# Performance work log

Measured on AMD Instinct MI355X. Metric: run time of the kernel, lower is better.

The kernel has to match this reference:

```python
import jax, jax.numpy as jnp
import numpy as np

B, N, C = 4, 2048, 1024
H = 16
D = C // H  # head_dim = 64

def setup_inputs() -> dict:
    key = jax.random.key(0)
    k1, k2, k3 = jax.random.split(key, 3)
    s = 1.0 / np.sqrt(C)
    x = jax.random.normal(k1, (B, N, C), dtype=jnp.float32)
    qkv_w = jax.random.normal(k2, (3 * C, C), dtype=jnp.float32) * s
    proj_w = jax.random.normal(k3, (C, C), dtype=jnp.float32) * s
    proj_b = jnp.zeros((C,), dtype=jnp.float32)
    return {"x": x, "qkv_w": qkv_w, "proj_w": proj_w, "proj_b": proj_b}

def reference(x, qkv_w, proj_w, proj_b):
    # qkv: torch Linear -> x @ W^T, no bias
    qkv = jnp.einsum('bnc,oc->bno', x, qkv_w)            # [B,N,3C]
    qkv = qkv.reshape(B, N, 3, H, D)
    q, k, v = qkv[:, :, 0], qkv[:, :, 1], qkv[:, :, 2]   # [B,N,H,D]
    scale = D ** -0.5
    scores = jnp.einsum('bqhd,bkhd->bhqk', q, k) * scale  # [B,H,N,N]
    causal = jnp.tril(jnp.ones((N, N), dtype=bool))
    scores = jnp.where(causal[None, None], scores, -jnp.inf)
    attn = jax.nn.softmax(scores, axis=-1)
    out = jnp.einsum('bhqk,bkhd->bqhd', attn, v).reshape(B, N, C)
    out = jnp.einsum('bnc,oc->bno', out, proj_w) + proj_b
    return out
```

## Files before the change

kernel.cpp:

```cpp
#include <hip/hip_runtime.h>
#include <math.h>

typedef __attribute__((ext_vector_type(8))) short short8;
typedef __attribute__((ext_vector_type(4))) short short4v;
typedef __attribute__((ext_vector_type(4))) float f32x4;
typedef __attribute__((ext_vector_type(4))) _Float16 half4v;

#define B_  4
#define N_  2048
#define C_  1024
#define H_  16
#define D_  64
#define TC3 3072

__device__ __forceinline__ short f2bf(float f) {
    unsigned u = __builtin_bit_cast(unsigned, f);
    u += 0x7fffu + ((u >> 16) & 1u);
    return (short)(u >> 16);
}

__device__ __forceinline__ half4v pack4h(float a, float b, float cc, float d) {
    auto lo = __builtin_amdgcn_cvt_pkrtz(a, b);
    auto hi = __builtin_amdgcn_cvt_pkrtz(cc, d);
    auto v4 = __builtin_shufflevector(lo, hi, 0, 1, 2, 3);
    return __builtin_bit_cast(half4v, v4);
}

__device__ __forceinline__ void gload16(const void* g, void* l) {
    __builtin_amdgcn_global_load_lds(
        (const __attribute__((address_space(1))) void*)g,
        (__attribute__((address_space(3))) void*)l, 16, 0, 0);
}

__global__ __launch_bounds__(256) void cast_to_bf16(const float* __restrict__ in,
                                                    short* __restrict__ out, int n8) {
    const int i = blockIdx.x * 256 + threadIdx.x;
    if (i >= n8) return;
    const float4 a = ((const float4*)in)[2 * i];
    const float4 b = ((const float4*)in)[2 * i + 1];
    short8 t;
    t[0] = f2bf(a.x); t[1] = f2bf(a.y); t[2] = f2bf(a.z); t[3] = f2bf(a.w);
    t[4] = f2bf(b.x); t[5] = f2bf(b.y); t[6] = f2bf(b.z); t[7] = f2bf(b.w);
    ((short8*)out)[i] = t;
}

#define GK 32

template <int MODE>
__global__ __launch_bounds__(256) void gemm_bf16(const short* __restrict__ A,
                                                 const short* __restrict__ Bw,
                                                 const float* __restrict__ bias,
                                                 short* __restrict__ Qb,
                                                 short* __restrict__ Kb,
                                                 _Float16* __restrict__ Vtb,
                                                 float* __restrict__ Fout,
                                                 int M, int Nn, int K) {
    __shared__ short smem[2 * 128 * GK];
    short* As = smem;
    short* Bs = smem + 128 * GK;

    const int tid = threadIdx.x;
    const int w = tid >> 6;
    const int ln = tid & 63;
    const int wm = w >> 1;
    const int wn = w & 1;
    const int c = ln & 15;
    const int g = ln >> 4;

    const int m0 = blockIdx.y * 128;
    const int n0 = blockIdx.x * 128;

    f32x4 acc[4][4];
#pragma unroll
    for (int m = 0; m < 4; ++m)
#pragma unroll
        for (int n = 0; n < 4; ++n) acc[m][n] = (f32x4){0.f, 0.f, 0.f, 0.f};

    const int lrow = ln >> 2;
    const int lseg = (ln & 3) * 8;

    for (int k0 = 0; k0 < K; k0 += GK) {
#pragma unroll
        for (int j = 0; j < 2; ++j) {
            const int row = w * 32 + j * 16 + lrow;
            gload16(A + (size_t)(m0 + row) * K + k0 + lseg, &As[(w * 32 + j * 16) * GK]);
            gload16(Bw + (size_t)(n0 + row) * K + k0 + lseg, &Bs[(w * 32 + j * 16) * GK]);
        }
        asm volatile("s_waitcnt vmcnt(0)" ::: "memory");
        __syncthreads();

        short8 aF[4], bF[4];
#pragma unroll
        for (int m = 0; m < 4; ++m)
            aF[m] = *(const short8*)&As[(wm * 64 + m * 16 + c) * GK + g * 8];
#pragma unroll
        for (int n = 0; n < 4; ++n)
            bF[n] = *(const short8*)&Bs[(wn * 64 + n * 16 + c) * GK + g * 8];
#pragma unroll
        for (int m = 0; m < 4; ++m)
#pragma unroll
            for (int n = 0; n < 4; ++n)
                acc[m][n] = __builtin_amdgcn_mfma_f32_16x16x32_bf16(aF[m], bF[n], acc[m][n], 0, 0, 0);
        __syncthreads();
    }

    if (MODE == 0) {
        const int mat = n0 >> 10;
        if (mat == 2) {
#pragma unroll
            for (int m = 0; m < 4; ++m) {
                const int row = m0 + wm * 64 + m * 16 + g * 4;
                const int b = row >> 11;
                const int nseq = row & 2047;
#pragma unroll
                for (int n = 0; n < 4; ++n) {
                    const int col = n0 + wn * 64 + n * 16 + c;
                    const int h = (col >> 6) & 15;
                    const int d = col & 63;
                    const half4v p = pack4h(acc[m][n][0], acc[m][n][1],
                                            acc[m][n][2], acc[m][n][3]);
                    *(half4v*)&Vtb[((size_t)(b * 16 + h) * 64 + d) * N_ + nseq] = p;
                }
            }
        } else {
            short* base = (mat == 0) ? Qb : Kb;
#pragma unroll
            for (int p = 0; p < 2; ++p) {
                __syncthreads();
                if (wn == p) {
#pragma unroll
                    for (int m = 0; m < 4; ++m)
#pragma unroll
                        for (int n = 0; n < 4; ++n)
#pragma unroll
                            for (int r = 0; r < 4; ++r)
                                smem[(wm * 64 + m * 16 + g * 4 + r) * 64 +
                                     (((n ^ g) * 16) + c)] = f2bf(acc[m][n][r]);
                }
                __syncthreads();
                const int row = tid >> 1;
                const int col0 = (tid & 1) * 32;
                const int gg = (row >> 2) & 3;
                const int grow = m0 + row;
                const int bb = grow >> 11, nseq = grow & 2047;
                const int h = ((n0 + p * 64) >> 6) & 15;
                short* dst = base + ((size_t)(bb * 16 + h) * N_ + nseq) * D_ + col0;
#pragma unroll
                for (int s16 = 0; s16 < 2; ++s16) {
                    const int Cb = col0 + s16 * 16;
                    const int ls_off = row * 64 + ((((Cb >> 4) ^ gg)) << 4);
                    *(short8*)(dst + s16 * 16) = *(const short8*)&smem[ls_off];
                    *(short8*)(dst + s16 * 16 + 8) = *(const short8*)&smem[ls_off + 8];
                }
            }
        }
    } else {
#pragma unroll
        for (int m = 0; m < 4; ++m) {
            const int row = m0 + wm * 64 + m * 16 + g * 4;
#pragma unroll
            for (int n = 0; n < 4; ++n) {
                const int col = n0 + wn * 64 + n * 16 + c;
                const float bv = bias[col];
#pragma unroll
                for (int r = 0; r < 4; ++r)
                    Fout[(size_t)(row + r) * Nn + col] = acc[m][n][r] + bv;
            }
        }
    }
}


__constant__ unsigned char CH_QT[40] = {0,1,2,3, 4,4, 5,5, 6,6, 7,7,
                                        8,8,8, 9,9,9, 10,10,10, 11,11,11,
                                        12,12,12,12, 13,13,13,13, 14,14,14,14, 15,15,15,15};
__constant__ unsigned char CH_C0[40] = {0,0,0,0, 0,1, 0,1, 0,1, 0,1,
                                        0,1,2, 0,1,2, 0,1,2, 0,1,2,
                                        0,1,2,3, 0,1,2,3, 0,1,2,3, 0,1,2,3};
__constant__ unsigned char CH_BASE[16] = {0,1,2,3,4,6,8,10,12,15,18,21,24,28,32,36};

__device__ __forceinline__ void stage_kv(const short* __restrict__ gK,
                                         const short* __restrict__ gV,
                                         short* KsB, short* VsB,
                                         int kt, int w, int lane) {
    const int sub = lane >> 3;
    const int sseg = (lane & 7) ^ sub;
#pragma unroll
    for (int j = 0; j < 2; ++j) {
        const int R0 = w * 16 + j * 8;
        const int row = R0 + sub;
        gload16(gK + (size_t)(kt * 64 + row) * D_ + sseg * 8, KsB + R0 * 64);
        gload16(gV + (size_t)row * N_ + kt * 64 + sseg * 8, VsB + R0 * 64);
    }
}

__global__ __launch_bounds__(256, 4) void attn_part(const short* __restrict__ Qb,
                                                    const short* __restrict__ Kb,
                                                    const _Float16* __restrict__ Vtb,
                                                    _Float16* __restrict__ Pp,
                                                    float* __restrict__ Lp) {
    __shared__ short Ks[2][64 * 64];
    __shared__ short Vts[2][64 * 64];

    const int bh = blockIdx.y;
    const int f = blockIdx.x;
    const int qt = CH_QT[f];
    const int kt0 = CH_C0[f] * 8;
    const int kt1 = min(kt0 + 8, 2 * qt + 2);

    const int tid = threadIdx.x;
    const int w = tid >> 6;
    const int lane = tid & 63;
    const int g = lane >> 4;
    const int c = lane & 15;
    const int swz = c & 7;
    const int rowmin = qt * 128 + w * 32;

    const short* gK = Kb + (size_t)bh * N_ * D_;
    const short* gV = (const short*)(Vtb + (size_t)bh * D_ * N_);

    short8 aQ[2][2];
    {
        const short* qb0 = Qb + ((size_t)bh * N_ + rowmin) * D_;
#pragma unroll
        for (int m = 0; m < 2; ++m) {
            aQ[m][0] = *(const short8*)(qb0 + (m * 16 + c) * D_ + g * 8);
            aQ[m][1] = *(const short8*)(qb0 + (m * 16 + c) * D_ + 32 + g * 8);
        }
    }

    f32x4 Oacc[2][4];
#pragma unroll
    for (int m = 0; m < 2; ++m)
#pragma unroll
        for (int nt = 0; nt < 4; ++nt) Oacc[m][nt] = (f32x4){0.f, 0.f, 0.f, 0.f};
    float ls[2] = {0.f, 0.f};

    stage_kv(gK, gV, Ks[0], Vts[0], kt0, w, lane);

    for (int kt = kt0; kt < kt1; ++kt) {
        const short* KsB = Ks[kt & 1];
        const short* VsB = Vts[kt & 1];
        asm volatile("s_waitcnt vmcnt(0)" ::: "memory");
        __syncthreads();
        if (kt + 1 < kt1)
            stage_kv(gK, gV, Ks[(kt + 1) & 1], Vts[(kt + 1) & 1], kt + 1, w, lane);

        const int kvb = kt * 64;
        if (kvb > rowmin + 31) continue;
        const bool needmask = (kvb + 63) > rowmin;

        f32x4 S[2][4];
#pragma unroll
        for (int m = 0; m < 2; ++m)
#pragma unroll
            for (int n = 0; n < 4; ++n) S[m][n] = (f32x4){0.f, 0.f, 0.f, 0.f};
#pragma unroll
        for (int n = 0; n < 4; ++n) {
            const short* kr = KsB + (n * 16 + c) * 64;
            const short8 bk0 = *(const short8*)(kr + (g ^ swz) * 8);
            const short8 bk1 = *(const short8*)(kr + ((4 + g) ^ swz) * 8);
#pragma unroll
            for (int m = 0; m < 2; ++m) {
                S[m][n] = __builtin_amdgcn_mfma_f32_16x16x32_bf16(bk0, aQ[m][0], S[m][n], 0, 0, 0);
                S[m][n] = __builtin_amdgcn_mfma_f32_16x16x32_bf16(bk1, aQ[m][1], S[m][n], 0, 0, 0);
            }
        }

        half4v Pb[2][4];
#pragma unroll
        for (int m = 0; m < 2; ++m) {
            const int qrow = rowmin + m * 16 + c;
#pragma unroll
            for (int n = 0; n < 4; ++n) {
                float p[4];
#pragma unroll
                for (int r = 0; r < 4; ++r) {
                    float pv = __expf(fmaf(S[m][n][r], 0.125f, -4.0f));
                    if (needmask && (kvb + n * 16 + g * 4 + r) > qrow) pv = 0.f;
                    ls[m] += pv;
                    p[r] = pv;
                }
                Pb[m][n] = pack4h(p[0], p[1], p[2], p[3]);
            }
        }

#pragma unroll
        for (int n = 0; n < 4; ++n) {
#pragma unroll
            for (int nt = 0; nt < 4; ++nt) {
                const int vrow = nt * 16 + c;
                const int vseg = (n * 2 + (g >> 1)) ^ swz;
                const half4v av = *(const half4v*)&VsB[vrow * 64 + vseg * 8 + (g & 1) * 4];
#pragma unroll
                for (int m = 0; m < 2; ++m)
                    Oacc[m][nt] = __builtin_amdgcn_mfma_f32_16x16x16f16(av, Pb[m][n], Oacc[m][nt], 0, 0, 0);
            }
        }
    }

#pragma unroll
    for (int m = 0; m < 2; ++m) {
        ls[m] += __shfl_xor(ls[m], 16);
        ls[m] += __shfl_xor(ls[m], 32);
    }

    const size_t slot = (size_t)bh * 40 + f;
    _Float16* dst = Pp + slot * (128 * 64);
#pragma unroll
    for (int m = 0; m < 2; ++m) {
        const int q = w * 32 + m * 16 + c;
#pragma unroll
        for (int nt = 0; nt < 4; ++nt) {
            const half4v o = pack4h(Oacc[m][nt][0], Oacc[m][nt][1],
                                    Oacc[m][nt][2], Oacc[m][nt][3]);
            *(half4v*)&dst[q * 64 + nt * 16 + g * 4] = o;
        }
        if (g == 0) Lp[slot * 128 + q] = ls[m];
    }
}

__global__ __launch_bounds__(256) void attn_reduce(const _Float16* __restrict__ Pp,
                                                   const float* __restrict__ Lp,
                                                   short* __restrict__ attnb) {
    const int qt = blockIdx.x;
    const int bh = blockIdx.y;
    const int b = bh >> 4, h = bh & 15;
    const int nc = (2 * qt + 2 + 7) / 8;
    const size_t slot0 = (size_t)bh * 40 + CH_BASE[qt];

    const int tid = threadIdx.x;
    const int q = tid >> 1;
    const int dh = (tid & 1) * 32;

    float acc[32];
#pragma unroll
    for (int i = 0; i < 32; ++i) acc[i] = 0.f;
    float l = 0.f;

    for (int cix = 0; cix < nc; ++cix) {
        const size_t s = slot0 + cix;
        l += Lp[s * 128 + q];
        const _Float16* p = Pp + s * (128 * 64) + q * 64 + dh;
#pragma unroll
        for (int v = 0; v < 4; ++v) {
            const half4v h4a = *(const half4v*)(p + v * 8);
            const half4v h4b = *(const half4v*)(p + v * 8 + 4);
#pragma unroll
            for (int r = 0; r < 4; ++r) {
                acc[v * 8 + r] += (float)h4a[r];
                acc[v * 8 + 4 + r] += (float)h4b[r];
            }
        }
    }

    const float inv = 1.0f / l;
    short* dst = attnb + (size_t)(b * N_ + qt * 128 + q) * C_ + h * D_ + dh;
#pragma unroll
    for (int v = 0; v < 4; ++v) {
        short8 o;
#pragma unroll
        for (int r = 0; r < 8; ++r) o[r] = f2bf(acc[v * 8 + r] * inv);
        *(short8*)(dst + v * 8) = o;
    }
}

extern "C" void kernel_launch(void* const* d_in, const int* in_sizes, int n_in,
                              void* d_out, int out_size, void* d_ws, size_t ws_size,
                              hipStream_t stream) {
    const float* x      = (const float*)d_in[0];
    const float* qkv_w  = (const float*)d_in[1];
    const float* proj_w = (const float*)d_in[2];
    const float* proj_b = (const float*)d_in[3];
    float* out = (float*)d_out;

    short* xb      = (short*)d_ws;
    short* qkv_wb  = xb + (size_t)B_ * N_ * C_;
    short* proj_wb = qkv_wb + (size_t)TC3 * C_;
    short* Qb      = proj_wb + (size_t)C_ * C_;
    short* Kb      = Qb + (size_t)B_ * H_ * N_ * D_;
    _Float16* Vtb  = (_Float16*)(Kb + (size_t)B_ * H_ * N_ * D_);
    short* attnb   = (short*)(Vtb + (size_t)B_ * H_ * N_ * D_);
    _Float16* Pp   = (_Float16*)(attnb + (size_t)B_ * N_ * C_);
    float* Lp      = (float*)(Pp + (size_t)64 * 40 * 128 * 64);

    const int M = B_ * N_;
    dim3 blk(256);

    cast_to_bf16<<<dim3((B_ * N_ * C_) / 8 / 256), blk, 0, stream>>>(x, xb, (B_ * N_ * C_) / 8);
    cast_to_bf16<<<dim3((TC3 * C_) / 8 / 256), blk, 0, stream>>>(qkv_w, qkv_wb, (TC3 * C_) / 8);
    cast_to_bf16<<<dim3((C_ * C_) / 8 / 256), blk, 0, stream>>>(proj_w, proj_wb, (C_ * C_) / 8);

    gemm_bf16<0><<<dim3(TC3 / 128, M / 128), blk, 0, stream>>>(
        xb, qkv_wb, nullptr, Qb, Kb, Vtb, nullptr, M, TC3, C_);

    attn_part<<<dim3(40, B_ * H_), blk, 0, stream>>>(Qb, Kb, Vtb, Pp, Lp);
    attn_reduce<<<dim3(N_ / 128, B_ * H_), blk, 0, stream>>>(Pp, Lp, attnb);

    gemm_bf16<1><<<dim3(C_ / 128, M / 128), blk, 0, stream>>>(
        attnb, proj_wb, proj_b, nullptr, nullptr, nullptr, out, M, C_, C_);
}
```

Baseline: 283.4 us.

## Merge cast kernels and deepen GEMM K-tile to 64 with XOR-swizzled LDS

Three fp32-to-bf16 cast launches become a single kernel that picks its source and destination by index range, removing two launches. The GEMM K-tile grows from 32 to 64, halving the number of barrier and wait rounds per output tile. The LDS layout gets an XOR swizzle on 16-byte segments so fragment reads avoid bank conflicts. The larger tile doubles LDS use per block, which could lower occupancy.

```diff
diff --git a/kernel.cpp b/kernel.cpp
--- a/kernel.cpp
+++ b/kernel.cpp
@@ -32,19 +32,31 @@
         (__attribute__((address_space(3))) void*)l, 16, 0, 0);
 }
 
-__global__ __launch_bounds__(256) void cast_to_bf16(const float* __restrict__ in,
-                                                    short* __restrict__ out, int n8) {
-    const int i = blockIdx.x * 256 + threadIdx.x;
-    if (i >= n8) return;
-    const float4 a = ((const float4*)in)[2 * i];
-    const float4 b = ((const float4*)in)[2 * i + 1];
+#define NX8  (B_ * N_ * C_ / 8)
+#define NQ8  (TC3 * C_ / 8)
+#define NP8  (C_ * C_ / 8)
+
+__global__ __launch_bounds__(256) void cast_all(const float* __restrict__ x,
+                                                const float* __restrict__ wq,
+                                                const float* __restrict__ wp,
+                                                short* __restrict__ xb,
+                                                short* __restrict__ wqb,
+                                                short* __restrict__ wpb) {
+    int i = blockIdx.x * 256 + threadIdx.x;
+    const float* src;
+    short* dst;
+    if (i < NX8) { src = x; dst = xb; }
+    else if (i < NX8 + NQ8) { i -= NX8; src = wq; dst = wqb; }
+    else { i -= NX8 + NQ8; src = wp; dst = wpb; }
+    const float4 a = ((const float4*)src)[2 * i];
+    const float4 b = ((const float4*)src)[2 * i + 1];
     short8 t;
     t[0] = f2bf(a.x); t[1] = f2bf(a.y); t[2] = f2bf(a.z); t[3] = f2bf(a.w);
     t[4] = f2bf(b.x); t[5] = f2bf(b.y); t[6] = f2bf(b.z); t[7] = f2bf(b.w);
-    ((short8*)out)[i] = t;
-}
-
-#define GK 32
+    ((short8*)dst)[i] = t;
+}
+
+#define GK 64
 
 template <int MODE>
 __global__ __launch_bounds__(256) void gemm_bf16(const short* __restrict__ A,
@@ -66,6 +78,7 @@
     const int wn = w & 1;
     const int c = ln & 15;
     const int g = ln >> 4;
+    const int c7 = c & 7;
 
     const int m0 = blockIdx.y * 128;
     const int n0 = blockIdx.x * 128;
@@ -76,31 +89,37 @@
 #pragma unroll
         for (int n = 0; n < 4; ++n) acc[m][n] = (f32x4){0.f, 0.f, 0.f, 0.f};
 
-    const int lrow = ln >> 2;
-    const int lseg = (ln & 3) * 8;
+    const int srow = ln >> 3;
+    const int sseg = (ln & 7) ^ srow;
 
     for (int k0 = 0; k0 < K; k0 += GK) {
 #pragma unroll
-        for (int j = 0; j < 2; ++j) {
-            const int row = w * 32 + j * 16 + lrow;
-            gload16(A + (size_t)(m0 + row) * K + k0 + lseg, &As[(w * 32 + j * 16) * GK]);
-            gload16(Bw + (size_t)(n0 + row) * K + k0 + lseg, &Bs[(w * 32 + j * 16) * GK]);
+        for (int j = 0; j < 4; ++j) {
+            const int R0 = w * 32 + j * 8;
+            const int row = R0 + srow;
+            gload16(A + (size_t)(m0 + row) * K + k0 + sseg * 8, &As[R0 * GK]);
+            gload16(Bw + (size_t)(n0 + row) * K + k0 + sseg * 8, &Bs[R0 * GK]);
         }
         asm volatile("s_waitcnt vmcnt(0)" ::: "memory");
         __syncthreads();
 
-        short8 aF[4], bF[4];
-#pragma unroll
-        for (int m = 0; m < 4; ++m)
-            aF[m] = *(const short8*)&As[(wm * 64 + m * 16 + c) * GK + g * 8];
-#pragma unroll
-        for (int n = 0; n < 4; ++n)
-            bF[n] = *(const short8*)&Bs[(wn * 64 + n * 16 + c) * GK + g * 8];
-#pragma unroll
-        for (int m = 0; m < 4; ++m)
+#pragma unroll
+        for (int kh = 0; kh < 2; ++kh) {
+            short8 aF[4], bF[4];
+#pragma unroll
+            for (int m = 0; m < 4; ++m)
+                aF[m] = *(const short8*)&As[(wm * 64 + m * 16 + c) * GK +
+                                            (((kh * 4 + g) ^ c7) * 8)];
 #pragma unroll
             for (int n = 0; n < 4; ++n)
-                acc[m][n] = __builtin_amdgcn_mfma_f32_16x16x32_bf16(aF[m], bF[n], acc[m][n], 0, 0, 0);
+                bF[n] = *(const short8*)&Bs[(wn * 64 + n * 16 + c) * GK +
+                                            (((kh * 4 + g) ^ c7) * 8)];
+#pragma unroll
+            for (int m = 0; m < 4; ++m)
+#pragma unroll
+                for (int n = 0; n < 4; ++n)
+                    acc[m][n] = __builtin_amdgcn_mfma_f32_16x16x32_bf16(aF[m], bF[n], acc[m][n], 0, 0, 0);
+        }
         __syncthreads();
     }
 
@@ -387,9 +406,8 @@
     const int M = B_ * N_;
     dim3 blk(256);
 
-    cast_to_bf16<<<dim3((B_ * N_ * C_) / 8 / 256), blk, 0, stream>>>(x, xb, (B_ * N_ * C_) / 8);
-    cast_to_bf16<<<dim3((TC3 * C_) / 8 / 256), blk, 0, stream>>>(qkv_w, qkv_wb, (TC3 * C_) / 8);
-    cast_to_bf16<<<dim3((C_ * C_) / 8 / 256), blk, 0, stream>>>(proj_w, proj_wb, (C_ * C_) / 8);
+    cast_all<<<dim3((NX8 + NQ8 + NP8) / 256), blk, 0, stream>>>(
+        x, qkv_w, proj_w, xb, qkv_wb, proj_wb);
 
     gemm_bf16<0><<<dim3(TC3 / 128, M / 128), blk, 0, stream>>>(
         xb, qkv_wb, nullptr, Qb, Kb, Vtb, nullptr, M, TC3, C_);
```

New measurement: 272.1 us. 4.0% less time.
